# Optimization experiments

Measured on AMD Instinct MI355X. Metric: run time of the kernel, lower is better.

The kernel has to match this reference:

```python
import jax, jax.numpy as jnp
import numpy as np

N = 50000      # nodes
E = 400000     # edges
D_IN = 128     # input node feature dim
H = 128        # hidden_dim == node_dim inside layers
E_DIM = 16     # edge_attr dim
L = 3          # num_layers


def setup_inputs() -> dict:
    key = jax.random.key(0)
    ks = jax.random.split(key, 8)
    s = 0.05
    return {
        "x": jax.random.normal(ks[0], (N, D_IN), jnp.float32),
        "edge_attr": jax.random.normal(ks[1], (E, E_DIM), jnp.float32),
        "edge_index": jax.random.randint(ks[2], (2, E), 0, N),
        # learned params (W stored [in, out], i.e. transpose of torch Linear.weight)
        "proj_W": jax.random.normal(ks[3], (D_IN, H), jnp.float32) * s,
        "proj_b": jnp.zeros((H,), jnp.float32),
        "msg_W1": jax.random.normal(ks[4], (L, 2 * H + E_DIM, H), jnp.float32) * s,
        "msg_b1": jnp.zeros((L, H), jnp.float32),
        "msg_W2": jax.random.normal(ks[5], (L, H, H), jnp.float32) * s,
        "msg_b2": jnp.zeros((L, H), jnp.float32),
        "upd_W": jax.random.normal(ks[6], (L, 2 * H, H), jnp.float32) * s,
        "upd_b": jnp.zeros((L, H), jnp.float32),
        "ln_g": jnp.ones((L, H), jnp.float32),
        "ln_b": jnp.zeros((L, H), jnp.float32),
        "out_g": jnp.ones((H,), jnp.float32),
        "out_b": jnp.zeros((H,), jnp.float32),
    }


def _layernorm(x, g, b, eps=1e-5):
    mu = jnp.mean(x, axis=-1, keepdims=True)
    var = jnp.mean((x - mu) ** 2, axis=-1, keepdims=True)
    return (x - mu) * jax.lax.rsqrt(var + eps) * g + b


def reference(x, edge_attr, edge_index, proj_W, proj_b, msg_W1, msg_b1,
              msg_W2, msg_b2, upd_W, upd_b, ln_g, ln_b, out_g, out_b):
    i_idx, j_idx = edge_index[0], edge_index[1]
    h = x @ proj_W + proj_b                       # [N, H]
    for l in range(L):                            # fixed small layer count
        # gather + message MLP: m_ij = relu(relu([h_i, h_j, e_ij] W1) W2)
        m_in = jnp.concatenate([h[i_idx], h[j_idx], edge_attr], axis=-1)  # [E, 2H+E_DIM]
        m = jax.nn.relu(m_in @ msg_W1[l] + msg_b1[l])
        m = jax.nn.relu(m @ msg_W2[l] + msg_b2[l])  # [E, H]
        # scatter-add aggregate to destination nodes (index_add_ on i_idx)
        agg = jax.ops.segment_sum(m, i_idx, num_segments=N)  # [N, H]
        # node update MLP + residual + LayerNorm (dropout p inactive in eval)
        out = jax.nn.relu(jnp.concatenate([h, agg], axis=-1) @ upd_W[l] + upd_b[l])
        h = _layernorm(out + h, ln_g[l], ln_b[l])
    h = _layernorm(h, out_g, out_b)
    return jnp.mean(h, axis=0)[None, :]           # global mean pool -> [1, H]
```

## Files before the change

### kernel.cpp

```cpp
#include <hip/hip_runtime.h>
#include <math.h>

#define N_NODES 50000
#define N_EDGES 400000
#define DIM_IN  128
#define H       128
#define E_DIM   16
#define NLAYERS 3

#define K1      272
#define K1P     288
#define HS      136
#define GSH     136
#define ETS     32
#define US      264
#define PS      136
#define FPS     132
#define MB      32
#define UMB     64
#define NT_E    (N_EDGES / MB)
#define NSB     ((N_NODES + 255) / 256)

typedef short    s16x8 __attribute__((ext_vector_type(8)));
typedef float    f32x4 __attribute__((ext_vector_type(4)));
typedef _Float16 f16x8 __attribute__((ext_vector_type(8)));
typedef __fp16   fp16x2 __attribute__((ext_vector_type(2)));
typedef unsigned u32x4 __attribute__((ext_vector_type(4)));

__device__ inline unsigned short f2bf(float f) {
    union { float f; unsigned u; } v; v.f = f;
    unsigned r = v.u + 0x7FFFu + ((v.u >> 16) & 1u);
    return (unsigned short)(r >> 16);
}
__device__ inline float bf2f(unsigned short u) {
    union { unsigned u; float f; } v; v.u = (unsigned)u << 16; return v.f;
}
__device__ inline unsigned pk2(float a, float b) {
    union { fp16x2 h; unsigned u; } v;
    v.h = __builtin_amdgcn_cvt_pkrtz(a, b);
    return v.u;
}
__device__ inline float f16lo(unsigned u) {
    union { unsigned short s; _Float16 h; } v; v.s = (unsigned short)(u & 0xffffu);
    return (float)v.h;
}
__device__ inline float f16hi(unsigned u) {
    union { unsigned short s; _Float16 h; } v; v.s = (unsigned short)(u >> 16);
    return (float)v.h;
}
__device__ inline float f16s(unsigned short s) {
    union { unsigned short s; _Float16 h; } v; v.s = s;
    return (float)v.h;
}

__global__ __launch_bounds__(256)
void convert_w1(const float* __restrict__ W1, unsigned short* __restrict__ W1t)
{
    const int o = blockIdx.x * 256 + threadIdx.x;
    const int l = o / (128 * K1P);
    const int r = o % (128 * K1P);
    const int n = r / K1P;
    const int k = r % K1P;
    const float v = (k < K1) ? W1[(size_t)l * K1 * H + (size_t)k * H + n] : 0.f;
    W1t[o] = f2bf(v);
}

__global__ __launch_bounds__(256)
void convert_w2(const float* __restrict__ W2, unsigned short* __restrict__ W2t)
{
    const int o = blockIdx.x * 256 + threadIdx.x;
    const int l = o / (H * H);
    const int r = o % (H * H);
    const int n = r / H;
    const int k = r % H;
    const int kp = (k & ~31) | ((k & 15) << 1) | ((k >> 4) & 1);
    union { _Float16 h; unsigned short s; } v;
    v.h = (_Float16)W2[(size_t)l * H * H + (size_t)k * H + n];
    W2t[(size_t)l * H * H + (size_t)n * H + kp] = v.s;
}

__global__ __launch_bounds__(256)
void convert_wu(const float* __restrict__ Wu, unsigned short* __restrict__ Wut)
{
    const int o = blockIdx.x * 256 + threadIdx.x;
    const int l = o / (H * 256);
    const int r = o % (H * 256);
    const int n = r / 256;
    const int k = r % 256;
    Wut[o] = f2bf(Wu[(size_t)l * 256 * H + (size_t)k * H + n]);
}

__global__ __launch_bounds__(256)
void convert_wp(const float* __restrict__ Wp, unsigned short* __restrict__ Wpt)
{
    const int o = blockIdx.x * 256 + threadIdx.x;
    const int n = o / H;
    const int k = o % H;
    Wpt[o] = f2bf(Wp[(size_t)k * H + n]);
}

__global__ __launch_bounds__(256)
void hist_kernel(const int* __restrict__ ei, int* __restrict__ hist)
{
    const int e = blockIdx.x * 256 + threadIdx.x;
    if (e < N_EDGES) atomicAdd(&hist[ei[e]], 1);
}

__global__ __launch_bounds__(256)
void blocksum_kernel(const int* __restrict__ hist, int* __restrict__ bsum)
{
    __shared__ int red[4];
    const int t = threadIdx.x;
    const int idx = blockIdx.x * 256 + t;
    int v = (idx < N_NODES) ? hist[idx] : 0;
#pragma unroll
    for (int off = 32; off > 0; off >>= 1) v += __shfl_xor(v, off, 64);
    if ((t & 63) == 0) red[t >> 6] = v;
    __syncthreads();
    if (t == 0) bsum[blockIdx.x] = red[0] + red[1] + red[2] + red[3];
}

__global__ __launch_bounds__(256)
void scan_bsum_kernel(const int* __restrict__ bsum, int* __restrict__ boff)
{
    __shared__ int s[256];
    const int t = threadIdx.x;
    const int v = (t < NSB) ? bsum[t] : 0;
    s[t] = v; __syncthreads();
    for (int off = 1; off < 256; off <<= 1) {
        const int u = (t >= off) ? s[t - off] : 0;
        __syncthreads();
        s[t] += u;
        __syncthreads();
    }
    if (t < NSB) boff[t] = s[t] - v;
}

__global__ __launch_bounds__(256)
void scan_final_kernel(const int* __restrict__ hist, const int* __restrict__ boff,
                       int* __restrict__ cursor)
{
    __shared__ int s[256];
    const int t = threadIdx.x;
    const int idx = blockIdx.x * 256 + t;
    const int v = (idx < N_NODES) ? hist[idx] : 0;
    s[t] = v; __syncthreads();
    for (int off = 1; off < 256; off <<= 1) {
        const int u = (t >= off) ? s[t - off] : 0;
        __syncthreads();
        s[t] += u;
        __syncthreads();
    }
    if (idx < N_NODES) cursor[idx] = boff[blockIdx.x] + s[t] - v;
}

__global__ __launch_bounds__(256)
void scatter_kernel(const int* __restrict__ ei, int* __restrict__ cursor,
                    const float* __restrict__ ea,
                    int* __restrict__ i_s, int* __restrict__ j_s,
                    unsigned short* __restrict__ eabf)
{
    const int e = blockIdx.x * 256 + threadIdx.x;
    if (e < N_EDGES) {
        const int d = ei[e];
        const int p = atomicAdd(&cursor[d], 1);
        i_s[p] = d;
        j_s[p] = ei[N_EDGES + e];
        const float4* src = (const float4*)(ea + (size_t)e * E_DIM);
        unsigned short o[16];
#pragma unroll
        for (int q = 0; q < 4; ++q) {
            const float4 v = src[q];
            o[q * 4 + 0] = f2bf(v.x);
            o[q * 4 + 1] = f2bf(v.y);
            o[q * 4 + 2] = f2bf(v.z);
            o[q * 4 + 3] = f2bf(v.w);
        }
        uint4* dst = (uint4*)(eabf + (size_t)p * E_DIM);
        dst[0] = *(const uint4*)&o[0];
        dst[1] = *(const uint4*)&o[8];
    }
}

__global__ __launch_bounds__(256)
void proj_mfma(const float* __restrict__ x, const unsigned short* __restrict__ Wpt,
               const float* __restrict__ b, unsigned short* __restrict__ hbf)
{
    __shared__ __align__(16) unsigned short A[MB][PS];
    const int tid = threadIdx.x;
    const int n0 = blockIdx.x * MB;
    const int wave = tid >> 6, lane = tid & 63, l15 = lane & 15, l4 = lane >> 4;
    const int colbase = wave * 32;

#pragma unroll
    for (int i = 0; i < 4; ++i) {
        const int f = tid + i * 256;
        const int row = f >> 5, c4 = f & 31;
        const int node = min(n0 + row, N_NODES - 1);
        const float4 v = *((const float4*)(x + (size_t)node * DIM_IN) + c4);
        unsigned short o[4] = { f2bf(v.x), f2bf(v.y), f2bf(v.z), f2bf(v.w) };
        *(uint2*)&A[row][c4 * 4] = *(const uint2*)o;
    }
    __syncthreads();

    f32x4 acc[2][2];
#pragma unroll
    for (int mt = 0; mt < 2; ++mt)
#pragma unroll
        for (int nt = 0; nt < 2; ++nt) acc[mt][nt] = (f32x4)0.f;

    for (int k = 0; k < DIM_IN; k += 32) {
        const s16x8 a0 = *(const s16x8*)&A[l15][k + l4 * 8];
        const s16x8 a1 = *(const s16x8*)&A[16 + l15][k + l4 * 8];
        const s16x8 b0 = *(const s16x8*)&Wpt[(size_t)(colbase + l15) * DIM_IN + k + l4 * 8];
        const s16x8 b1 = *(const s16x8*)&Wpt[(size_t)(colbase + 16 + l15) * DIM_IN + k + l4 * 8];
        acc[0][0] = __builtin_amdgcn_mfma_f32_16x16x32_bf16(a0, b0, acc[0][0], 0, 0, 0);
        acc[0][1] = __builtin_amdgcn_mfma_f32_16x16x32_bf16(a0, b1, acc[0][1], 0, 0, 0);
        acc[1][0] = __builtin_amdgcn_mfma_f32_16x16x32_bf16(a1, b0, acc[1][0], 0, 0, 0);
        acc[1][1] = __builtin_amdgcn_mfma_f32_16x16x32_bf16(a1, b1, acc[1][1], 0, 0, 0);
    }

    const float bi0 = b[colbase + l15], bi1 = b[colbase + 16 + l15];
#pragma unroll
    for (int mt = 0; mt < 2; ++mt)
#pragma unroll
        for (int r = 0; r < 4; ++r) {
            const int row = mt * 16 + l4 * 4 + r;
            const int n = n0 + row;
            if (n < N_NODES) {
                hbf[(size_t)n * H + colbase + l15]      = f2bf(acc[mt][0][r] + bi0);
                hbf[(size_t)n * H + colbase + 16 + l15] = f2bf(acc[mt][1][r] + bi1);
            }
        }
}

__global__ __launch_bounds__(256)
void premul(const unsigned short* __restrict__ hbf,
            const unsigned short* __restrict__ W1t,
            unsigned short* __restrict__ Pa, unsigned short* __restrict__ Pb)
{
    __shared__ __align__(16) unsigned short A[MB][PS];
    const int tid = threadIdx.x;
    const int n0 = blockIdx.x * MB;
    const int wave = tid >> 6, lane = tid & 63, l15 = lane & 15, l4 = lane >> 4;
    const int colbase = wave * 32;

#pragma unroll
    for (int i = 0; i < 2; ++i) {
        const int f = tid + i * 256;
        const int row = f >> 4, c = f & 15;
        const int node = min(n0 + row, N_NODES - 1);
        const uint4 v = *((const uint4*)(hbf + (size_t)node * H) + c);
        *(uint4*)&A[row][c * 8] = v;
    }
    __syncthreads();

    f32x4 aa[2][2], ab[2][2];
#pragma unroll
    for (int mt = 0; mt < 2; ++mt)
#pragma unroll
        for (int nt = 0; nt < 2; ++nt) { aa[mt][nt] = (f32x4)0.f; ab[mt][nt] = (f32x4)0.f; }

#pragma unroll
    for (int kt = 0; kt < 4; ++kt) {
        const s16x8 a0 = *(const s16x8*)&A[l15][kt * 32 + l4 * 8];
        const s16x8 a1 = *(const s16x8*)&A[16 + l15][kt * 32 + l4 * 8];
        const s16x8 wa0 = *(const s16x8*)&W1t[(size_t)(colbase + l15) * K1P + kt * 32 + l4 * 8];
        const s16x8 wa1 = *(const s16x8*)&W1t[(size_t)(colbase + 16 + l15) * K1P + kt * 32 + l4 * 8];
        const s16x8 wb0 = *(const s16x8*)&W1t[(size_t)(colbase + l15) * K1P + 128 + kt * 32 + l4 * 8];
        const s16x8 wb1 = *(const s16x8*)&W1t[(size_t)(colbase + 16 + l15) * K1P + 128 + kt * 32 + l4 * 8];
        aa[0][0] = __builtin_amdgcn_mfma_f32_16x16x32_bf16(a0, wa0, aa[0][0], 0, 0, 0);
        aa[0][1] = __builtin_amdgcn_mfma_f32_16x16x32_bf16(a0, wa1, aa[0][1], 0, 0, 0);
        aa[1][0] = __builtin_amdgcn_mfma_f32_16x16x32_bf16(a1, wa0, aa[1][0], 0, 0, 0);
        aa[1][1] = __builtin_amdgcn_mfma_f32_16x16x32_bf16(a1, wa1, aa[1][1], 0, 0, 0);
        ab[0][0] = __builtin_amdgcn_mfma_f32_16x16x32_bf16(a0, wb0, ab[0][0], 0, 0, 0);
        ab[0][1] = __builtin_amdgcn_mfma_f32_16x16x32_bf16(a0, wb1, ab[0][1], 0, 0, 0);
        ab[1][0] = __builtin_amdgcn_mfma_f32_16x16x32_bf16(a1, wb0, ab[1][0], 0, 0, 0);
        ab[1][1] = __builtin_amdgcn_mfma_f32_16x16x32_bf16(a1, wb1, ab[1][1], 0, 0, 0);
    }

#pragma unroll
    for (int mt = 0; mt < 2; ++mt)
#pragma unroll
        for (int r = 0; r < 4; ++r) {
            const int row = mt * 16 + l4 * 4 + r;
            const int n = n0 + row;
            if (n < N_NODES) {
                *(unsigned*)&Pa[(size_t)n * H + colbase + 2 * l15] = pk2(aa[mt][0][r], aa[mt][1][r]);
                *(unsigned*)&Pb[(size_t)n * H + colbase + 2 * l15] = pk2(ab[mt][0][r], ab[mt][1][r]);
            }
        }
}

__global__ __launch_bounds__(256, 4)
void edge_kernel(const unsigned short* __restrict__ Pa,
                 const unsigned short* __restrict__ Pb,
                 const unsigned short* __restrict__ eabf,
                 const int*   __restrict__ i_s,
                 const int*   __restrict__ j_s,
                 const unsigned short* __restrict__ W1t,
                 const float* __restrict__ b1,
                 const unsigned short* __restrict__ W2t,
                 const float* __restrict__ b2,
                 float*       __restrict__ agg)
{
    __shared__ __align__(16) unsigned short Gs[MB * GSH];
    __shared__ __align__(16) unsigned short Et[MB * ETS];
    __shared__ __align__(16) unsigned short Hid[MB * HS];
    __shared__ __align__(16) unsigned short Mbf[MB * HS];
    __shared__ int idxbuf[2][MB];

    const int tid  = threadIdx.x;
    const int wave = tid >> 6;
    const int lane = tid & 63;
    const int l15  = lane & 15;
    const int l4   = lane >> 4;
    const int colbase = wave * 32;

    const int sl_e = tid >> 4;
    const int sl_c = tid & 15;

    f16x8 w2f[2][4];
    s16x8 w1cf[2];
#pragma unroll
    for (int kt = 0; kt < 4; ++kt) {
        w2f[0][kt] = *(const f16x8*)&W2t[(size_t)(colbase + l15) * H + kt * 32 + l4 * 8];
        w2f[1][kt] = *(const f16x8*)&W2t[(size_t)(colbase + 16 + l15) * H + kt * 32 + l4 * 8];
    }
    w1cf[0] = *(const s16x8*)&W1t[(size_t)(colbase + l15) * K1P + 256 + l4 * 8];
    w1cf[1] = *(const s16x8*)&W1t[(size_t)(colbase + 16 + l15) * K1P + 256 + l4 * 8];
    const float b1c0 = b1[colbase + l15], b1c1 = b1[colbase + 16 + l15];
    const float b2c0 = b2[colbase + l15], b2c1 = b2[colbase + 16 + l15];

    const int rc   = tid & 127;
    const int rh   = tid >> 7;
    const int kpc  = (rc & ~31) | ((rc & 15) << 1) | ((rc >> 4) & 1);
    const int rr0  = rh * 16;

    int t = blockIdx.x;
    if (t >= NT_E) return;

    {
#pragma unroll
        for (int i = 0; i < 2; ++i) {
            const int e  = sl_e + i * 16;
            const int ni = i_s[t * MB + e];
            const int nj = j_s[t * MB + e];
            union { uint4 u; f16x8 h; } a, b, s;
            a.u = *((const uint4*)(Pa + (size_t)ni * H) + sl_c);
            b.u = *((const uint4*)(Pb + (size_t)nj * H) + sl_c);
            s.h = a.h + b.h;
            *(uint4*)&Gs[e * GSH + sl_c * 8] = s.u;
        }
        if (tid < 64) {
            const u32x4 ve = __builtin_nontemporal_load((const u32x4*)eabf + (size_t)t * 64 + tid);
            *(u32x4*)&Et[(tid >> 1) * ETS + (tid & 1) * 8] = ve;
        } else if (tid < 128) {
            const int tt = tid - 64;
            const uint4 z = {0, 0, 0, 0};
            *(uint4*)&Et[(tt >> 1) * ETS + 16 + (tt & 1) * 8] = z;
        }
        if (tid < MB) idxbuf[0][tid] = i_s[t * MB + tid];
    }
    __syncthreads();

    int p = 0;
    for (; t < NT_E; t += gridDim.x, p ^= 1) {
        const int t1 = t + gridDim.x;

        uint4 pfa[2], pfb[2];
        u32x4 pfe = {0, 0, 0, 0};
        int   pfi = 0;
        if (t1 < NT_E) {
#pragma unroll
            for (int i = 0; i < 2; ++i) {
                const int e = sl_e + i * 16;
                pfa[i] = *((const uint4*)(Pa + (size_t)i_s[t1 * MB + e] * H) + sl_c);
                pfb[i] = *((const uint4*)(Pb + (size_t)j_s[t1 * MB + e] * H) + sl_c);
            }
            if (tid < 64) pfe = __builtin_nontemporal_load((const u32x4*)eabf + (size_t)t1 * 64 + tid);
            if (tid < MB) pfi = i_s[t1 * MB + tid];
        }

        f32x4 acc[2][2];
#pragma unroll
        for (int mt = 0; mt < 2; ++mt) {
            acc[mt][0] = (f32x4)(b1c0);
            acc[mt][1] = (f32x4)(b1c1);
        }
        {
            const s16x8 a0 = *(const s16x8*)&Et[l15 * ETS + l4 * 8];
            const s16x8 a1 = *(const s16x8*)&Et[(16 + l15) * ETS + l4 * 8];
            acc[0][0] = __builtin_amdgcn_mfma_f32_16x16x32_bf16(a0, w1cf[0], acc[0][0], 0, 0, 0);
            acc[0][1] = __builtin_amdgcn_mfma_f32_16x16x32_bf16(a0, w1cf[1], acc[0][1], 0, 0, 0);
            acc[1][0] = __builtin_amdgcn_mfma_f32_16x16x32_bf16(a1, w1cf[0], acc[1][0], 0, 0, 0);
            acc[1][1] = __builtin_amdgcn_mfma_f32_16x16x32_bf16(a1, w1cf[1], acc[1][1], 0, 0, 0);
        }

#pragma unroll
        for (int mt = 0; mt < 2; ++mt)
#pragma unroll
            for (int r = 0; r < 4; ++r) {
                const int row = mt * 16 + l4 * 4 + r;
                const unsigned gv = *(const unsigned*)&Gs[row * GSH + colbase + 2 * l15];
                const unsigned hh = pk2(fmaxf(acc[mt][0][r] + f16lo(gv), 0.f),
                                        fmaxf(acc[mt][1][r] + f16hi(gv), 0.f));
                *(unsigned*)&Hid[row * HS + colbase + 2 * l15] = hh;
            }
        __syncthreads();

        if (t1 < NT_E) {
#pragma unroll
            for (int i = 0; i < 2; ++i) {
                const int e = sl_e + i * 16;
                union { uint4 u; f16x8 h; } a, b, s;
                a.u = pfa[i]; b.u = pfb[i];
                s.h = a.h + b.h;
                *(uint4*)&Gs[e * GSH + sl_c * 8] = s.u;
            }
            if (tid < 64)
                *(u32x4*)&Et[(tid >> 1) * ETS + (tid & 1) * 8] = pfe;
            if (tid < MB) idxbuf[p ^ 1][tid] = pfi;
        }

#pragma unroll
        for (int mt = 0; mt < 2; ++mt) {
            acc[mt][0] = (f32x4)(b2c0);
            acc[mt][1] = (f32x4)(b2c1);
        }
#pragma unroll
        for (int kt = 0; kt < 4; ++kt) {
            const f16x8 a0 = *(const f16x8*)&Hid[l15 * HS + kt * 32 + l4 * 8];
            const f16x8 a1 = *(const f16x8*)&Hid[(16 + l15) * HS + kt * 32 + l4 * 8];
            acc[0][0] = __builtin_amdgcn_mfma_f32_16x16x32_f16(a0, w2f[0][kt], acc[0][0], 0, 0, 0);
            acc[0][1] = __builtin_amdgcn_mfma_f32_16x16x32_f16(a0, w2f[1][kt], acc[0][1], 0, 0, 0);
            acc[1][0] = __builtin_amdgcn_mfma_f32_16x16x32_f16(a1, w2f[0][kt], acc[1][0], 0, 0, 0);
            acc[1][1] = __builtin_amdgcn_mfma_f32_16x16x32_f16(a1, w2f[1][kt], acc[1][1], 0, 0, 0);
        }

#pragma unroll
        for (int mt = 0; mt < 2; ++mt)
#pragma unroll
            for (int r = 0; r < 4; ++r) {
                const int row = mt * 16 + l4 * 4 + r;
                const unsigned mm = pk2(fmaxf(acc[mt][0][r], 0.f),
                                        fmaxf(acc[mt][1][r], 0.f));
                *(unsigned*)&Mbf[row * HS + colbase + 2 * l15] = mm;
            }
        __syncthreads();

        {
            const int* idxp = idxbuf[p];
            int cur = idxp[rr0];
            bool bnd = true;
            float s = 0.f;
            for (int r = rr0; r < rr0 + 16; ++r) {
                const int d = idxp[r];
                if (d != cur) {
                    float* addr = &agg[(size_t)cur * H + rc];
                    if (bnd) atomicAdd(addr, s); else *addr = s;
                    s = 0.f; cur = d; bnd = false;
                }
                s += f16s(Mbf[r * HS + kpc]);
            }
            atomicAdd(&agg[(size_t)cur * H + rc], s);
        }
    }
}

__global__ __launch_bounds__(256, 3)
void update_mfma(unsigned short* __restrict__ hbf, float* __restrict__ agg,
                 const unsigned short* __restrict__ Wut, const float* __restrict__ b,
                 const float* __restrict__ g, const float* __restrict__ bln,
                 const int rezero)
{
    __shared__ __align__(16) unsigned short A[UMB][US];
    float* Afp = (float*)&A[0][0];

    const int tid = threadIdx.x;
    const int n0 = blockIdx.x * UMB;
    const int wave = tid >> 6, lane = tid & 63, l15 = lane & 15, l4 = lane >> 4;
    const int colbase = wave * 32;

    s16x8 bf0[8], bf1[8];
#pragma unroll
    for (int kt = 0; kt < 8; ++kt) {
        bf0[kt] = *(const s16x8*)&Wut[(size_t)(colbase + l15) * 256 + kt * 32 + l4 * 8];
        bf1[kt] = *(const s16x8*)&Wut[(size_t)(colbase + 16 + l15) * 256 + kt * 32 + l4 * 8];
    }

#pragma unroll
    for (int i = 0; i < 4; ++i) {
        const int f = tid + i * 256;
        const int row = f >> 4, c = f & 15;
        const int node = min(n0 + row, N_NODES - 1);
        const uint4 v = *((const uint4*)(hbf + (size_t)node * H) + c);
        *(uint4*)&A[row][c * 8] = v;
    }
#pragma unroll
    for (int i = 0; i < 8; ++i) {
        const int f = tid + i * 256;
        const int row = f >> 5, c4 = f & 31;
        const int node = min(n0 + row, N_NODES - 1);
        float4* ap = (float4*)(agg + (size_t)node * H) + c4;
        const float4 v = *ap;
        if (rezero && n0 + row < N_NODES) {
            const float4 z = {0.f, 0.f, 0.f, 0.f};
            *ap = z;
        }
        unsigned short o[4] = { f2bf(v.x), f2bf(v.y), f2bf(v.z), f2bf(v.w) };
        *(uint2*)&A[row][128 + c4 * 4] = *(const uint2*)o;
    }
    __syncthreads();

    f32x4 acc[4][2];
#pragma unroll
    for (int mt = 0; mt < 4; ++mt) { acc[mt][0] = (f32x4)0.f; acc[mt][1] = (f32x4)0.f; }

#pragma unroll
    for (int kt = 0; kt < 8; ++kt) {
#pragma unroll
        for (int mt = 0; mt < 4; ++mt) {
            const s16x8 a = *(const s16x8*)&A[mt * 16 + l15][kt * 32 + l4 * 8];
            acc[mt][0] = __builtin_amdgcn_mfma_f32_16x16x32_bf16(a, bf0[kt], acc[mt][0], 0, 0, 0);
            acc[mt][1] = __builtin_amdgcn_mfma_f32_16x16x32_bf16(a, bf1[kt], acc[mt][1], 0, 0, 0);
        }
    }
    __syncthreads();

    {
        const float bi0 = b[colbase + l15], bi1 = b[colbase + 16 + l15];
#pragma unroll
        for (int mt = 0; mt < 4; ++mt)
#pragma unroll
            for (int r = 0; r < 4; ++r) {
                const int row = mt * 16 + l4 * 4 + r;
                Afp[row * FPS + colbase + l15]      = fmaxf(acc[mt][0][r] + bi0, 0.f);
                Afp[row * FPS + colbase + 16 + l15] = fmaxf(acc[mt][1][r] + bi1, 0.f);
            }
    }
    __syncthreads();

    {
        const int rrow = tid >> 2;
        const int rq   = tid & 3;
        const int c0   = rq * 32;
        const int nn   = n0 + rrow;
        if (nn < N_NODES) {
            float v[32];
            const unsigned short* hrow = hbf + (size_t)nn * H + c0;
            float s = 0.f;
#pragma unroll
            for (int i = 0; i < 8; ++i) {
                const float4 a = *(const float4*)&Afp[rrow * FPS + c0 + i * 4];
                const ushort4 hu = *(const ushort4*)&hrow[i * 4];
                v[i * 4 + 0] = a.x + bf2f(hu.x);
                v[i * 4 + 1] = a.y + bf2f(hu.y);
                v[i * 4 + 2] = a.z + bf2f(hu.z);
                v[i * 4 + 3] = a.w + bf2f(hu.w);
                s += v[i * 4 + 0] + v[i * 4 + 1] + v[i * 4 + 2] + v[i * 4 + 3];
            }
            s += __shfl_xor(s, 1, 64);
            s += __shfl_xor(s, 2, 64);
            const float mu = s * (1.f / 128.f);
            float vs = 0.f;
#pragma unroll
            for (int i = 0; i < 32; ++i) { const float d = v[i] - mu; vs += d * d; }
            vs += __shfl_xor(vs, 1, 64);
            vs += __shfl_xor(vs, 2, 64);
            const float inv = rsqrtf(vs * (1.f / 128.f) + 1e-5f);
#pragma unroll
            for (int i = 0; i < 8; ++i) {
                const float4 gv = *(const float4*)&g[c0 + i * 4];
                const float4 bv = *(const float4*)&bln[c0 + i * 4];
                unsigned short o[4] = {
                    f2bf((v[i * 4 + 0] - mu) * inv * gv.x + bv.x),
                    f2bf((v[i * 4 + 1] - mu) * inv * gv.y + bv.y),
                    f2bf((v[i * 4 + 2] - mu) * inv * gv.z + bv.z),
                    f2bf((v[i * 4 + 3] - mu) * inv * gv.w + bv.w)
                };
                *(uint2*)&hbf[(size_t)nn * H + c0 + i * 4] = *(const uint2*)o;
            }
        }
    }
}

__global__ __launch_bounds__(256)
void final_kernel(const unsigned short* __restrict__ hbf,
                  const float* __restrict__ g, const float* __restrict__ b,
                  float* __restrict__ out)
{
    __shared__ float red[4][128];
    const int tid = threadIdx.x;
    const int wave = tid >> 6, lane = tid & 63;
    const float g0 = g[lane], g1 = g[64 + lane];
    const float b0 = b[lane], b1 = b[64 + lane];
    float a0 = 0.f, a1 = 0.f;

    for (int n = blockIdx.x * 4 + wave; n < N_NODES; n += gridDim.x * 4) {
        const float v0 = bf2f(hbf[(size_t)n * H + lane]);
        const float v1 = bf2f(hbf[(size_t)n * H + 64 + lane]);
        float s = v0 + v1;
#pragma unroll
        for (int off = 32; off > 0; off >>= 1) s += __shfl_xor(s, off, 64);
        const float mu = s * (1.f / 128.f);
        const float d0 = v0 - mu, d1 = v1 - mu;
        float vs = d0 * d0 + d1 * d1;
#pragma unroll
        for (int off = 32; off > 0; off >>= 1) vs += __shfl_xor(vs, off, 64);
        const float inv = rsqrtf(vs * (1.f / 128.f) + 1e-5f);
        a0 += d0 * inv * g0 + b0;
        a1 += d1 * inv * g1 + b1;
    }
    red[wave][lane]      = a0;
    red[wave][64 + lane] = a1;
    __syncthreads();
    if (wave == 0) {
        const float s0 = red[0][lane] + red[1][lane] + red[2][lane] + red[3][lane];
        const float s1 = red[0][64 + lane] + red[1][64 + lane] + red[2][64 + lane] + red[3][64 + lane];
        atomicAdd(&out[lane],      s0 * (1.f / N_NODES));
        atomicAdd(&out[64 + lane], s1 * (1.f / N_NODES));
    }
}

extern "C" void kernel_launch(void* const* d_in, const int* in_sizes, int n_in,
                              void* d_out, int out_size, void* d_ws, size_t ws_size,
                              hipStream_t stream)
{
    const float* x         = (const float*)d_in[0];
    const float* edge_attr = (const float*)d_in[1];
    const int*   edge_idx  = (const int*)  d_in[2];
    const float* proj_W    = (const float*)d_in[3];
    const float* proj_b    = (const float*)d_in[4];
    const float* msg_W1    = (const float*)d_in[5];
    const float* msg_b1    = (const float*)d_in[6];
    const float* msg_W2    = (const float*)d_in[7];
    const float* msg_b2    = (const float*)d_in[8];
    const float* upd_W     = (const float*)d_in[9];
    const float* upd_b     = (const float*)d_in[10];
    const float* ln_g      = (const float*)d_in[11];
    const float* ln_b      = (const float*)d_in[12];
    const float* out_g     = (const float*)d_in[13];
    const float* out_b     = (const float*)d_in[14];
    float* out = (float*)d_out;

    char* w = (char*)d_ws;
    float* agg = (float*)w;                   w += (size_t)N_NODES * H * 4;
    unsigned short* hbf  = (unsigned short*)w; w += (size_t)N_NODES * H * 2;
    unsigned short* Pa   = (unsigned short*)w; w += (size_t)N_NODES * H * 2;
    unsigned short* Pb   = (unsigned short*)w; w += (size_t)N_NODES * H * 2;
    unsigned short* eabf = (unsigned short*)w; w += (size_t)N_EDGES * E_DIM * 2;
    unsigned short* W1t  = (unsigned short*)w; w += (size_t)NLAYERS * H * K1P * 2;
    unsigned short* W2t  = (unsigned short*)w; w += (size_t)NLAYERS * H * H * 2;
    unsigned short* Wut  = (unsigned short*)w; w += (size_t)NLAYERS * H * 256 * 2;
    unsigned short* Wpt  = (unsigned short*)w; w += (size_t)H * DIM_IN * 2;
    int* hist   = (int*)w;                    w += (size_t)N_NODES * 4;
    int* cursor = (int*)w;                    w += (size_t)N_NODES * 4;
    int* bsum   = (int*)w;                    w += (size_t)256 * 4;
    int* boff   = (int*)w;                    w += (size_t)256 * 4;
    int* i_s    = (int*)w;                    w += (size_t)N_EDGES * 4;
    int* j_s    = (int*)w;                    w += (size_t)N_EDGES * 4;

    convert_w1<<<(NLAYERS * H * K1P) / 256, 256, 0, stream>>>(msg_W1, W1t);
    convert_w2<<<(NLAYERS * H * H) / 256, 256, 0, stream>>>(msg_W2, W2t);
    convert_wu<<<(NLAYERS * H * 256) / 256, 256, 0, stream>>>(upd_W, Wut);
    convert_wp<<<(H * DIM_IN) / 256, 256, 0, stream>>>(proj_W, Wpt);

    hipMemsetAsync(hist, 0, (size_t)N_NODES * 4, stream);
    hipMemsetAsync(agg, 0, (size_t)N_NODES * H * sizeof(float), stream);
    hist_kernel<<<(N_EDGES + 255) / 256, 256, 0, stream>>>(edge_idx, hist);
    blocksum_kernel<<<NSB, 256, 0, stream>>>(hist, bsum);
    scan_bsum_kernel<<<1, 256, 0, stream>>>(bsum, boff);
    scan_final_kernel<<<NSB, 256, 0, stream>>>(hist, boff, cursor);
    scatter_kernel<<<(N_EDGES + 255) / 256, 256, 0, stream>>>(edge_idx, cursor, edge_attr, i_s, j_s, eabf);

    const int nblk = (N_NODES + MB - 1) / MB;
    proj_mfma<<<nblk, 256, 0, stream>>>(x, Wpt, proj_b, hbf);

    const int ublk = (N_NODES + UMB - 1) / UMB;
    for (int l = 0; l < NLAYERS; ++l) {
        premul<<<nblk, 256, 0, stream>>>(hbf, W1t + (size_t)l * H * K1P, Pa, Pb);
        edge_kernel<<<1024, 256, 0, stream>>>(
            Pa, Pb, eabf, i_s, j_s,
            W1t + (size_t)l * H * K1P, msg_b1 + (size_t)l * H,
            W2t + (size_t)l * H * H,   msg_b2 + (size_t)l * H, agg);
        update_mfma<<<ublk, 256, 0, stream>>>(
            hbf, agg, Wut + (size_t)l * H * 256, upd_b + (size_t)l * H,
            ln_g + (size_t)l * H, ln_b + (size_t)l * H,
            (l < NLAYERS - 1) ? 1 : 0);
    }

    hipMemsetAsync(out, 0, H * sizeof(float), stream);
    final_kernel<<<256, 256, 0, stream>>>(hbf, out_g, out_b, out);
}
```

Measured before the change: 483.9 us.

## Fuse next-layer premul and final layernorm-pool into update kernel

The node update kernel now runs the next layer's premultiplication (h·W1 halves into Pa/Pb) straight from the freshly normalized rows held in shared memory, which removes the separate premul launches for layers 1 and 2 and their re-read of hbf. In the last layer it applies the output layernorm in registers and writes per-block column sums, which a small deterministic reduce kernel then combines. This replaces final_kernel, its atomics and the output memset. The cost is extra shared memory and registers in update_mfma, which may lower occupancy.

```diff
diff --git a/kernel.cpp b/kernel.cpp
--- a/kernel.cpp
+++ b/kernel.cpp
@@ -15,9 +15,12 @@
 #define ETS     32
 #define US      264
 #define PS      136
+#define AHS     136
 #define FPS     132
 #define MB      32
 #define UMB     64
+#define UBLK    ((N_NODES + UMB - 1) / UMB)
+#define GPR     800
 #define NT_E    (N_EDGES / MB)
 #define NSB     ((N_NODES + 255) / 256)
 
@@ -472,9 +475,14 @@
 void update_mfma(unsigned short* __restrict__ hbf, float* __restrict__ agg,
                  const unsigned short* __restrict__ Wut, const float* __restrict__ b,
                  const float* __restrict__ g, const float* __restrict__ bln,
-                 const int rezero)
+                 const unsigned short* __restrict__ W1n,
+                 unsigned short* __restrict__ Pa, unsigned short* __restrict__ Pb,
+                 const float* __restrict__ og, const float* __restrict__ ob,
+                 float* __restrict__ gpart,
+                 const int mode)
 {
     __shared__ __align__(16) unsigned short A[UMB][US];
+    __shared__ __align__(16) unsigned short Ah[UMB][AHS];
     float* Afp = (float*)&A[0][0];
 
     const int tid = threadIdx.x;
@@ -504,7 +512,7 @@
         const int node = min(n0 + row, N_NODES - 1);
         float4* ap = (float4*)(agg + (size_t)node * H) + c4;
         const float4 v = *ap;
-        if (rezero && n0 + row < N_NODES) {
+        if (mode == 0 && n0 + row < N_NODES) {
             const float4 z = {0.f, 0.f, 0.f, 0.f};
             *ap = z;
         }
@@ -569,58 +577,150 @@
             vs += __shfl_xor(vs, 1, 64);
             vs += __shfl_xor(vs, 2, 64);
             const float inv = rsqrtf(vs * (1.f / 128.f) + 1e-5f);
-#pragma unroll
-            for (int i = 0; i < 8; ++i) {
-                const float4 gv = *(const float4*)&g[c0 + i * 4];
-                const float4 bv = *(const float4*)&bln[c0 + i * 4];
-                unsigned short o[4] = {
-                    f2bf((v[i * 4 + 0] - mu) * inv * gv.x + bv.x),
-                    f2bf((v[i * 4 + 1] - mu) * inv * gv.y + bv.y),
-                    f2bf((v[i * 4 + 2] - mu) * inv * gv.z + bv.z),
-                    f2bf((v[i * 4 + 3] - mu) * inv * gv.w + bv.w)
-                };
-                *(uint2*)&hbf[(size_t)nn * H + c0 + i * 4] = *(const uint2*)o;
-            }
-        }
-    }
-}
-
-__global__ __launch_bounds__(256)
-void final_kernel(const unsigned short* __restrict__ hbf,
-                  const float* __restrict__ g, const float* __restrict__ b,
-                  float* __restrict__ out)
-{
-    __shared__ float red[4][128];
-    const int tid = threadIdx.x;
-    const int wave = tid >> 6, lane = tid & 63;
-    const float g0 = g[lane], g1 = g[64 + lane];
-    const float b0 = b[lane], b1 = b[64 + lane];
-    float a0 = 0.f, a1 = 0.f;
-
-    for (int n = blockIdx.x * 4 + wave; n < N_NODES; n += gridDim.x * 4) {
-        const float v0 = bf2f(hbf[(size_t)n * H + lane]);
-        const float v1 = bf2f(hbf[(size_t)n * H + 64 + lane]);
-        float s = v0 + v1;
-#pragma unroll
-        for (int off = 32; off > 0; off >>= 1) s += __shfl_xor(s, off, 64);
-        const float mu = s * (1.f / 128.f);
-        const float d0 = v0 - mu, d1 = v1 - mu;
-        float vs = d0 * d0 + d1 * d1;
-#pragma unroll
-        for (int off = 32; off > 0; off >>= 1) vs += __shfl_xor(vs, off, 64);
-        const float inv = rsqrtf(vs * (1.f / 128.f) + 1e-5f);
-        a0 += d0 * inv * g0 + b0;
-        a1 += d1 * inv * g1 + b1;
-    }
-    red[wave][lane]      = a0;
-    red[wave][64 + lane] = a1;
+
+            if (mode == 0) {
+#pragma unroll
+                for (int i = 0; i < 8; ++i) {
+                    const float4 gv = *(const float4*)&g[c0 + i * 4];
+                    const float4 bv = *(const float4*)&bln[c0 + i * 4];
+                    unsigned short o[4] = {
+                        f2bf((v[i * 4 + 0] - mu) * inv * gv.x + bv.x),
+                        f2bf((v[i * 4 + 1] - mu) * inv * gv.y + bv.y),
+                        f2bf((v[i * 4 + 2] - mu) * inv * gv.z + bv.z),
+                        f2bf((v[i * 4 + 3] - mu) * inv * gv.w + bv.w)
+                    };
+                    *(uint2*)&hbf[(size_t)nn * H + c0 + i * 4] = *(const uint2*)o;
+                    *(uint2*)&Ah[rrow][c0 + i * 4] = *(const uint2*)o;
+                }
+            } else {
+                float h1[32];
+                float s2 = 0.f;
+#pragma unroll
+                for (int i = 0; i < 8; ++i) {
+                    const float4 gv = *(const float4*)&g[c0 + i * 4];
+                    const float4 bv = *(const float4*)&bln[c0 + i * 4];
+                    h1[i * 4 + 0] = (v[i * 4 + 0] - mu) * inv * gv.x + bv.x;
+                    h1[i * 4 + 1] = (v[i * 4 + 1] - mu) * inv * gv.y + bv.y;
+                    h1[i * 4 + 2] = (v[i * 4 + 2] - mu) * inv * gv.z + bv.z;
+                    h1[i * 4 + 3] = (v[i * 4 + 3] - mu) * inv * gv.w + bv.w;
+                    s2 += h1[i * 4 + 0] + h1[i * 4 + 1] + h1[i * 4 + 2] + h1[i * 4 + 3];
+                }
+                s2 += __shfl_xor(s2, 1, 64);
+                s2 += __shfl_xor(s2, 2, 64);
+                const float mu2 = s2 * (1.f / 128.f);
+                float vs2 = 0.f;
+#pragma unroll
+                for (int i = 0; i < 32; ++i) { const float d = h1[i] - mu2; vs2 += d * d; }
+                vs2 += __shfl_xor(vs2, 1, 64);
+                vs2 += __shfl_xor(vs2, 2, 64);
+                const float inv2 = rsqrtf(vs2 * (1.f / 128.f) + 1e-5f);
+#pragma unroll
+                for (int i = 0; i < 8; ++i) {
+                    const float4 gv = *(const float4*)&og[c0 + i * 4];
+                    const float4 bv = *(const float4*)&ob[c0 + i * 4];
+                    float4 o;
+                    o.x = (h1[i * 4 + 0] - mu2) * inv2 * gv.x + bv.x;
+                    o.y = (h1[i * 4 + 1] - mu2) * inv2 * gv.y + bv.y;
+                    o.z = (h1[i * 4 + 2] - mu2) * inv2 * gv.z + bv.z;
+                    o.w = (h1[i * 4 + 3] - mu2) * inv2 * gv.w + bv.w;
+                    *(float4*)&Afp[rrow * FPS + c0 + i * 4] = o;
+                }
+            }
+        } else if (mode == 1) {
+            const float4 z = {0.f, 0.f, 0.f, 0.f};
+#pragma unroll
+            for (int i = 0; i < 8; ++i)
+                *(float4*)&Afp[rrow * FPS + c0 + i * 4] = z;
+        }
+    }
+
+    if (mode == 0) {
+        __syncthreads();
+        {
+            s16x8 wf0[4], wf1[4];
+#pragma unroll
+            for (int kt = 0; kt < 4; ++kt) {
+                wf0[kt] = *(const s16x8*)&W1n[(size_t)(colbase + l15) * K1P + kt * 32 + l4 * 8];
+                wf1[kt] = *(const s16x8*)&W1n[(size_t)(colbase + 16 + l15) * K1P + kt * 32 + l4 * 8];
+            }
+            f32x4 pacc[4][2];
+#pragma unroll
+            for (int mt = 0; mt < 4; ++mt) { pacc[mt][0] = (f32x4)0.f; pacc[mt][1] = (f32x4)0.f; }
+#pragma unroll
+            for (int kt = 0; kt < 4; ++kt)
+#pragma unroll
+                for (int mt = 0; mt < 4; ++mt) {
+                    const s16x8 a = *(const s16x8*)&Ah[mt * 16 + l15][kt * 32 + l4 * 8];
+                    pacc[mt][0] = __builtin_amdgcn_mfma_f32_16x16x32_bf16(a, wf0[kt], pacc[mt][0], 0, 0, 0);
+                    pacc[mt][1] = __builtin_amdgcn_mfma_f32_16x16x32_bf16(a, wf1[kt], pacc[mt][1], 0, 0, 0);
+                }
+#pragma unroll
+            for (int mt = 0; mt < 4; ++mt)
+#pragma unroll
+                for (int r = 0; r < 4; ++r) {
+                    const int row = mt * 16 + l4 * 4 + r;
+                    const int n = n0 + row;
+                    if (n < N_NODES)
+                        *(unsigned*)&Pa[(size_t)n * H + colbase + 2 * l15] = pk2(pacc[mt][0][r], pacc[mt][1][r]);
+                }
+        }
+        {
+            s16x8 wf0[4], wf1[4];
+#pragma unroll
+            for (int kt = 0; kt < 4; ++kt) {
+                wf0[kt] = *(const s16x8*)&W1n[(size_t)(colbase + l15) * K1P + 128 + kt * 32 + l4 * 8];
+                wf1[kt] = *(const s16x8*)&W1n[(size_t)(colbase + 16 + l15) * K1P + 128 + kt * 32 + l4 * 8];
+            }
+            f32x4 pacc[4][2];
+#pragma unroll
+            for (int mt = 0; mt < 4; ++mt) { pacc[mt][0] = (f32x4)0.f; pacc[mt][1] = (f32x4)0.f; }
+#pragma unroll
+            for (int kt = 0; kt < 4; ++kt)
+#pragma unroll
+                for (int mt = 0; mt < 4; ++mt) {
+                    const s16x8 a = *(const s16x8*)&Ah[mt * 16 + l15][kt * 32 + l4 * 8];
+                    pacc[mt][0] = __builtin_amdgcn_mfma_f32_16x16x32_bf16(a, wf0[kt], pacc[mt][0], 0, 0, 0);
+                    pacc[mt][1] = __builtin_amdgcn_mfma_f32_16x16x32_bf16(a, wf1[kt], pacc[mt][1], 0, 0, 0);
+                }
+#pragma unroll
+            for (int mt = 0; mt < 4; ++mt)
+#pragma unroll
+                for (int r = 0; r < 4; ++r) {
+                    const int row = mt * 16 + l4 * 4 + r;
+                    const int n = n0 + row;
+                    if (n < N_NODES)
+                        *(unsigned*)&Pb[(size_t)n * H + colbase + 2 * l15] = pk2(pacc[mt][0][r], pacc[mt][1][r]);
+                }
+        }
+    } else {
+        __syncthreads();
+        const int col  = tid & 127;
+        const int half = tid >> 7;
+        float s = 0.f;
+        for (int r = half * 32; r < half * 32 + 32; ++r)
+            s += Afp[r * FPS + col];
+        float* colsum = (float*)&Ah[0][0];
+        if (half) colsum[col] = s;
+        __syncthreads();
+        if (!half)
+            gpart[(size_t)col * GPR + blockIdx.x] = s + colsum[col];
+    }
+}
+
+__global__ __launch_bounds__(256)
+void final_reduce(const float* __restrict__ gpart, float* __restrict__ out)
+{
+    __shared__ float red[4];
+    const int c = blockIdx.x;
+    const int t = threadIdx.x;
+    const int wave = t >> 6, lane = t & 63;
+    float s = 0.f;
+    for (int r = t; r < UBLK; r += 256) s += gpart[(size_t)c * GPR + r];
+#pragma unroll
+    for (int off = 32; off > 0; off >>= 1) s += __shfl_xor(s, off, 64);
+    if (lane == 0) red[wave] = s;
     __syncthreads();
-    if (wave == 0) {
-        const float s0 = red[0][lane] + red[1][lane] + red[2][lane] + red[3][lane];
-        const float s1 = red[0][64 + lane] + red[1][64 + lane] + red[2][64 + lane] + red[3][64 + lane];
-        atomicAdd(&out[lane],      s0 * (1.f / N_NODES));
-        atomicAdd(&out[64 + lane], s1 * (1.f / N_NODES));
-    }
+    if (t == 0) out[c] = (red[0] + red[1] + red[2] + red[3]) * (1.f / N_NODES);
 }
 
 extern "C" void kernel_launch(void* const* d_in, const int* in_sizes, int n_in,
@@ -654,6 +754,7 @@
     unsigned short* W2t  = (unsigned short*)w; w += (size_t)NLAYERS * H * H * 2;
     unsigned short* Wut  = (unsigned short*)w; w += (size_t)NLAYERS * H * 256 * 2;
     unsigned short* Wpt  = (unsigned short*)w; w += (size_t)H * DIM_IN * 2;
+    float* gpart = (float*)w;                 w += (size_t)H * GPR * 4;
     int* hist   = (int*)w;                    w += (size_t)N_NODES * 4;
     int* cursor = (int*)w;                    w += (size_t)N_NODES * 4;
     int* bsum   = (int*)w;                    w += (size_t)256 * 4;
@@ -676,20 +777,20 @@
 
     const int nblk = (N_NODES + MB - 1) / MB;
     proj_mfma<<<nblk, 256, 0, stream>>>(x, Wpt, proj_b, hbf);
-
-    const int ublk = (N_NODES + UMB - 1) / UMB;
+    premul<<<nblk, 256, 0, stream>>>(hbf, W1t, Pa, Pb);
+
     for (int l = 0; l < NLAYERS; ++l) {
-        premul<<<nblk, 256, 0, stream>>>(hbf, W1t + (size_t)l * H * K1P, Pa, Pb);
         edge_kernel<<<1024, 256, 0, stream>>>(
             Pa, Pb, eabf, i_s, j_s,
             W1t + (size_t)l * H * K1P, msg_b1 + (size_t)l * H,
             W2t + (size_t)l * H * H,   msg_b2 + (size_t)l * H, agg);
-        update_mfma<<<ublk, 256, 0, stream>>>(
+        update_mfma<<<UBLK, 256, 0, stream>>>(
             hbf, agg, Wut + (size_t)l * H * 256, upd_b + (size_t)l * H,
             ln_g + (size_t)l * H, ln_b + (size_t)l * H,
-            (l < NLAYERS - 1) ? 1 : 0);
-    }
-
-    hipMemsetAsync(out, 0, H * sizeof(float), stream);
-    final_kernel<<<256, 256, 0, stream>>>(hbf, out_g, out_b, out);
-}
+            W1t + (size_t)((l < NLAYERS - 1) ? (l + 1) : 0) * H * K1P,
+            Pa, Pb, out_g, out_b, gpart,
+            (l < NLAYERS - 1) ? 0 : 1);
+    }
+
+    final_reduce<<<H, 256, 0, stream>>>(gpart, out);
+}
```

Result: faster. 454.4 us (-6.1%).
